# Optimization experiments

Hardware: AMD Instinct MI355X
Metric: run time of the kernel (lower is better)

## Reference

```python
import jax, jax.numpy as jnp
import numpy as np

NV = 8192
NH = 4096

def setup_inputs() -> dict:
    key = jax.random.key(0)
    ks = jax.random.split(key, 8)
    return {
        "muvTE": jax.random.normal(ks[0], (NV,), dtype=jnp.float32),
        "varvhTE": jax.random.normal(ks[1], (NH, NV), dtype=jnp.float32),
        "varh_diagTE": jax.random.normal(ks[2], (NH,), dtype=jnp.float32),
        # strictly positive variances, bounded away from zero
        "varh_diag": jax.random.uniform(ks[3], (NH,), dtype=jnp.float32) + 0.5,
        "muh": jax.random.normal(ks[4], (NH,), dtype=jnp.float32),
        "varvh": jax.random.normal(ks[5], (NH, NV), dtype=jnp.float32),
        "muhTE": jax.random.normal(ks[6], (NH,), dtype=jnp.float32),
        "varvbarTE": jax.random.normal(ks[7], (), dtype=jnp.float32),
    }


def reference(muvTE, varvhTE, varh_diagTE, varh_diag, muh, varvh, muhTE, varvbarTE):
    nv = muvTE.shape[0]
    inv = 1.0 / varh_diag                      # diag(varh_inv), [nh]
    inv_muh = inv * muh                        # varh_inv @ muh, [nh]
    # varh_inv @ varhTE @ varh_inv @ muh  (all diagonal scalings)
    ivTEv_muh = inv * (varh_diagTE * inv_muh)  # [nh]

    # bTE: [nv]
    bTE = (muvTE
           - varvhTE.T @ inv_muh
           + varvh.T @ ivTEv_muh
           - varvh.T @ (inv * muhTE))

    # wtTE = -varh_inv varhTE varh_inv varvh + varh_inv varvhTE : [nh, nv]
    d = inv * varh_diagTE * inv                # [nh]
    wtTE = -d[:, None] * varvh + inv[:, None] * varvhTE

    # trace of sig2TEmat without materializing [nv, nv]:
    # tr(A^T diag(s) B) = sum(A * (s[:,None] * B))
    tr = (jnp.sum(varvhTE * (inv[:, None] * varvh))
          - jnp.sum(varvh * (d[:, None] * varvh))
          + jnp.sum(varvh * (inv[:, None] * varvhTE)))
    sig2TE = (varvbarTE - tr) / nv

    return (bTE, wtTE, sig2TE, muhTE, varh_diagTE)
```

## Files before the change

### kernel.cpp

```cpp
#include <hip/hip_runtime.h>

#define NV 8192
#define NH 4096
#define TPB 256
#define HPB 16
#define HCH (NH / HPB)
#define ROW4 (NV / 4)
#define VBLK (ROW4 / TPB)
#define NPART (VBLK * HCH)
#define CH 4
#define NCHUNK (HPB / CH)

typedef float f32x4 __attribute__((ext_vector_type(4)));

#define OFF_B   ((size_t)0)
#define OFF_WT  ((size_t)NV)
#define OFF_SIG ((size_t)NV + (size_t)NH * (size_t)NV)
#define OFF_MUH (OFF_SIG + 1)
#define OFF_VHD (OFF_MUH + NH)

__global__ __launch_bounds__(TPB) void init_k(
    const float* __restrict__ muvTE,
    const float* __restrict__ varh_diagTE,
    const float* __restrict__ muhTE,
    float* __restrict__ out)
{
    int i = blockIdx.x * TPB + threadIdx.x;
    if (i < NV) out[OFF_B + i] = muvTE[i];
    if (i < NH) {
        out[OFF_MUH + i] = muhTE[i];
        out[OFF_VHD + i] = varh_diagTE[i];
    }
}

__global__ __launch_bounds__(TPB, 4) void main_k(
    const float4* __restrict__ varvhTE4,
    const float4* __restrict__ varvh4,
    const float* __restrict__ varh_diagTE,
    const float* __restrict__ varh_diag,
    const float* __restrict__ muh,
    const float* __restrict__ muhTE,
    float* __restrict__ out,
    float* __restrict__ tr_partial)
{
    __shared__ float4 coef_s[HPB];
    const int t  = threadIdx.x;
    const int h0 = blockIdx.y * HPB;

    if (t < HPB) {
        int h = h0 + t;
        float inv  = 1.0f / varh_diag[h];
        float vte  = varh_diagTE[h];
        float d    = inv * vte * inv;
        float m    = muh[h];
        coef_s[t] = make_float4(inv, inv * m, d * m - inv * muhTE[h], d);
    }
    __syncthreads();

    const int v4 = blockIdx.x * TPB + t;
    f32x4* wt4 = (f32x4*)(out + OFF_WT);
    const size_t base = (size_t)h0 * ROW4 + (size_t)v4;

    float bx = 0.f, by = 0.f, bz = 0.f, bw = 0.f;
    float tr = 0.f;

    float4 aTE_b[2][CH], a_b[2][CH];

    #pragma unroll
    for (int r = 0; r < CH; ++r) {
        size_t idx = base + (size_t)r * ROW4;
        aTE_b[0][r] = varvhTE4[idx];
        a_b[0][r]   = varvh4[idx];
    }

    #pragma unroll
    for (int c = 0; c < NCHUNK; ++c) {
        const int cur = c & 1, nxt = cur ^ 1;

        if (c + 1 < NCHUNK) {
            #pragma unroll
            for (int r = 0; r < CH; ++r) {
                size_t idx = base + (size_t)((c + 1) * CH + r) * ROW4;
                aTE_b[nxt][r] = varvhTE4[idx];
                a_b[nxt][r]   = varvh4[idx];
            }
        }

        #pragma unroll
        for (int r = 0; r < CH; ++r) {
            float4 cf  = coef_s[c * CH + r];
            float4 aTE = aTE_b[cur][r];
            float4 a   = a_b[cur][r];
            size_t idx = base + (size_t)(c * CH + r) * ROW4;

            f32x4 w;
            w.x = cf.x * aTE.x - cf.w * a.x;
            w.y = cf.x * aTE.y - cf.w * a.y;
            w.z = cf.x * aTE.z - cf.w * a.z;
            w.w = cf.x * aTE.w - cf.w * a.w;
            __builtin_nontemporal_store(w, &wt4[idx]);

            bx += cf.z * a.x - cf.y * aTE.x;
            by += cf.z * a.y - cf.y * aTE.y;
            bz += cf.z * a.z - cf.y * aTE.z;
            bw += cf.z * a.w - cf.y * aTE.w;

            float dot = aTE.x * a.x + aTE.y * a.y + aTE.z * a.z + aTE.w * a.w;
            float sq  = a.x * a.x + a.y * a.y + a.z * a.z + a.w * a.w;
            tr += 2.0f * cf.x * dot - cf.w * sq;
        }
    }

    int v = v4 * 4;
    atomicAdd(&out[OFF_B + v + 0], bx);
    atomicAdd(&out[OFF_B + v + 1], by);
    atomicAdd(&out[OFF_B + v + 2], bz);
    atomicAdd(&out[OFF_B + v + 3], bw);

    for (int off = 32; off > 0; off >>= 1)
        tr += __shfl_down(tr, off);
    __shared__ float wsum[TPB / 64];
    if ((t & 63) == 0) wsum[t >> 6] = tr;
    __syncthreads();
    if (t == 0) {
        float s = wsum[0] + wsum[1] + wsum[2] + wsum[3];
        tr_partial[blockIdx.y * VBLK + blockIdx.x] = s;
    }
}

__global__ __launch_bounds__(TPB) void fin_k(
    const float* __restrict__ tr_partial,
    const float* __restrict__ varvbarTE,
    float* __restrict__ out)
{
    int t = threadIdx.x;
    float s = 0.f;
    for (int i = t; i < NPART; i += TPB) s += tr_partial[i];
    for (int off = 32; off > 0; off >>= 1)
        s += __shfl_down(s, off);
    __shared__ float wsum[TPB / 64];
    if ((t & 63) == 0) wsum[t >> 6] = s;
    __syncthreads();
    if (t == 0) {
        float tr = wsum[0] + wsum[1] + wsum[2] + wsum[3];
        out[OFF_SIG] = (varvbarTE[0] - tr) / (float)NV;
    }
}

extern "C" void kernel_launch(void* const* d_in, const int* in_sizes, int n_in,
                              void* d_out, int out_size, void* d_ws, size_t ws_size,
                              hipStream_t stream) {
    const float* muvTE       = (const float*)d_in[0];
    const float* varvhTE     = (const float*)d_in[1];
    const float* varh_diagTE = (const float*)d_in[2];
    const float* varh_diag   = (const float*)d_in[3];
    const float* muh         = (const float*)d_in[4];
    const float* varvh       = (const float*)d_in[5];
    const float* muhTE       = (const float*)d_in[6];
    const float* varvbarTE   = (const float*)d_in[7];
    float* out        = (float*)d_out;
    float* tr_partial = (float*)d_ws;

    init_k<<<NV / TPB, TPB, 0, stream>>>(muvTE, varh_diagTE, muhTE, out);
    main_k<<<dim3(VBLK, HCH), TPB, 0, stream>>>(
        (const float4*)varvhTE, (const float4*)varvh,
        varh_diagTE, varh_diag, muh, muhTE, out, tr_partial);
    fin_k<<<1, TPB, 0, stream>>>(tr_partial, varvbarTE, out);
}
```

Measured before the change: 359.9 us.

## Issue all row loads up front and halve rows per block

Replaces the chunked double-buffered load loop with a single batch that loads all rows per thread into registers before computing. A compiler barrier keeps the loads grouped. Rows per block drop from 16 to 8, doubling the grid. This raises memory-level parallelism per thread and adds more blocks, but doubles the atomic adds into b and the partial-trace entries.

Result: faster. 349.1 us (-3.0%).

```diff
diff --git a/kernel.cpp b/kernel.cpp
--- a/kernel.cpp
+++ b/kernel.cpp
@@ -3,13 +3,11 @@
 #define NV 8192
 #define NH 4096
 #define TPB 256
-#define HPB 16
+#define HPB 8
 #define HCH (NH / HPB)
 #define ROW4 (NV / 4)
 #define VBLK (ROW4 / TPB)
 #define NPART (VBLK * HCH)
-#define CH 4
-#define NCHUNK (HPB / CH)
 
 typedef float f32x4 __attribute__((ext_vector_type(4)));
 
@@ -61,54 +59,40 @@
     f32x4* wt4 = (f32x4*)(out + OFF_WT);
     const size_t base = (size_t)h0 * ROW4 + (size_t)v4;
 
+    float4 aTE_r[HPB], a_r[HPB];
+    #pragma unroll
+    for (int r = 0; r < HPB; ++r) {
+        size_t idx = base + (size_t)r * ROW4;
+        aTE_r[r] = varvhTE4[idx];
+        a_r[r]   = varvh4[idx];
+    }
+    asm volatile("" ::: "memory");
+
     float bx = 0.f, by = 0.f, bz = 0.f, bw = 0.f;
     float tr = 0.f;
 
-    float4 aTE_b[2][CH], a_b[2][CH];
+    #pragma unroll
+    for (int r = 0; r < HPB; ++r) {
+        float4 cf  = coef_s[r];
+        float4 aTE = aTE_r[r];
+        float4 a   = a_r[r];
+        size_t idx = base + (size_t)r * ROW4;
 
-    #pragma unroll
-    for (int r = 0; r < CH; ++r) {
-        size_t idx = base + (size_t)r * ROW4;
-        aTE_b[0][r] = varvhTE4[idx];
-        a_b[0][r]   = varvh4[idx];
-    }
+        f32x4 w;
+        w.x = cf.x * aTE.x - cf.w * a.x;
+        w.y = cf.x * aTE.y - cf.w * a.y;
+        w.z = cf.x * aTE.z - cf.w * a.z;
+        w.w = cf.x * aTE.w - cf.w * a.w;
+        __builtin_nontemporal_store(w, &wt4[idx]);
 
-    #pragma unroll
-    for (int c = 0; c < NCHUNK; ++c) {
-        const int cur = c & 1, nxt = cur ^ 1;
+        bx += cf.z * a.x - cf.y * aTE.x;
+        by += cf.z * a.y - cf.y * aTE.y;
+        bz += cf.z * a.z - cf.y * aTE.z;
+        bw += cf.z * a.w - cf.y * aTE.w;
 
-        if (c + 1 < NCHUNK) {
-            #pragma unroll
-            for (int r = 0; r < CH; ++r) {
-                size_t idx = base + (size_t)((c + 1) * CH + r) * ROW4;
-                aTE_b[nxt][r] = varvhTE4[idx];
-                a_b[nxt][r]   = varvh4[idx];
-            }
-        }
-
-        #pragma unroll
-        for (int r = 0; r < CH; ++r) {
-            float4 cf  = coef_s[c * CH + r];
-            float4 aTE = aTE_b[cur][r];
-            float4 a   = a_b[cur][r];
-            size_t idx = base + (size_t)(c * CH + r) * ROW4;
-
-            f32x4 w;
-            w.x = cf.x * aTE.x - cf.w * a.x;
-            w.y = cf.x * aTE.y - cf.w * a.y;
-            w.z = cf.x * aTE.z - cf.w * a.z;
-            w.w = cf.x * aTE.w - cf.w * a.w;
-            __builtin_nontemporal_store(w, &wt4[idx]);
-
-            bx += cf.z * a.x - cf.y * aTE.x;
-            by += cf.z * a.y - cf.y * aTE.y;
-            bz += cf.z * a.z - cf.y * aTE.z;
-            bw += cf.z * a.w - cf.y * aTE.w;
-
-            float dot = aTE.x * a.x + aTE.y * a.y + aTE.z * a.z + aTE.w * a.w;
-            float sq  = a.x * a.x + a.y * a.y + a.z * a.z + a.w * a.w;
-            tr += 2.0f * cf.x * dot - cf.w * sq;
-        }
+        float dot = aTE.x * a.x + aTE.y * a.y + aTE.z * a.z + aTE.w * a.w;
+        float sq  = a.x * a.x + a.y * a.y + a.z * a.z + a.w * a.w;
+        tr += 2.0f * cf.x * dot - cf.w * sq;
     }
 
     int v = v4 * 4;
```
